# Performance work log

Measured on AMD Instinct MI355X. Metric: run time of the kernel, lower is better.

Reference implementation:

```python
import jax, jax.numpy as jnp
import numpy as np

N = 100000
F_IN = 128
HID = 64
N_CLS = 40
E = 1600000


def gcn_conv(x, src, dst, W, b, n_nodes):
    """PyG GCNConv: add self-loops, symmetric deg^{-1/2} normalization.

    Self-loop contribution handled analytically (norm_ii = 1/deg_i) so we
    never concatenate self-loop edges.
    """
    h = x @ W                                      # [N, out]
    # in-degree including self-loop
    deg = jax.ops.segment_sum(jnp.ones((src.shape[0],), x.dtype), dst,
                              num_segments=n_nodes) + 1.0
    dinv = jax.lax.rsqrt(deg)                      # deg^{-1/2}, [N]
    norm = dinv[src] * dinv[dst]                   # [E]
    msg = h[src] * norm[:, None]                   # [E, out] gather + scale
    agg = jax.ops.segment_sum(msg, dst, num_segments=n_nodes)
    return agg + h * (dinv * dinv)[:, None] + b


def setup_inputs() -> dict:
    key = jax.random.key(0)
    k1, k2, k3, k4, k5, k6 = jax.random.split(key, 6)
    x = jax.random.normal(k1, (N, F_IN), dtype=jnp.float32)
    edge_index = jax.random.randint(k2, (2, E), 0, N, dtype=jnp.int64)
    W1 = jax.random.normal(k3, (F_IN, HID), dtype=jnp.float32) / np.sqrt(F_IN)
    b1 = jnp.zeros((HID,), jnp.float32)
    W2 = jax.random.normal(k4, (HID, N_CLS), dtype=jnp.float32) / np.sqrt(HID)
    b2 = jnp.zeros((N_CLS,), jnp.float32)
    return {"x": x, "edge_index": edge_index, "W1": W1, "b1": b1,
            "W2": W2, "b2": b2}


def reference(x, edge_index, W1, b1, W2, b2):
    src, dst = edge_index[0], edge_index[1]
    h = jax.nn.relu(gcn_conv(x, src, dst, W1, b1, N))
    # dropout p=0.5 is identity at inference (training=False)
    out = gcn_conv(h, src, dst, W2, b2, N)
    return out
```

## Files before the change

kernel.cpp:

```cpp
#include <hip/hip_runtime.h>
#include <stdint.h>

#define NN    100000
#define FIN   128
#define HIDN  64
#define NCLS  40
#define NE    1600000
#define NBUCK ((NN + 255) / 256)
#define EPB   4096
#define NEB   ((NE + EPB - 1) / EPB)

typedef unsigned int uint32;
typedef __attribute__((ext_vector_type(8))) short short8v;
typedef __attribute__((ext_vector_type(4))) float f32x4;

static __device__ __forceinline__ unsigned short f2bf(float f) {
  uint32 u = __float_as_uint(f);
  u = (u + 0x7fffu + ((u >> 16) & 1u)) >> 16;
  return (unsigned short)u;
}
static __device__ __forceinline__ uint32 pack2(float lo, float hi) {
  return (uint32)f2bf(lo) | ((uint32)f2bf(hi) << 16);
}
static __device__ __forceinline__ float bf_lo(uint32 v) {
  return __uint_as_float(v << 16);
}
static __device__ __forceinline__ float bf_hi(uint32 v) {
  return __uint_as_float(v & 0xFFFF0000u);
}
static __device__ __forceinline__ f32x4 mfma_bf16(uint4 a, uint4 b, f32x4 c) {
  short8v av = __builtin_bit_cast(short8v, a);
  short8v bv = __builtin_bit_cast(short8v, b);
  return __builtin_amdgcn_mfma_f32_16x16x32_bf16(av, bv, c, 0, 0, 0);
}

static __device__ __forceinline__ int perm_col(int z) {
  return 4 * (z >> 3) + ((z & 7) >> 1) + 16 * (z & 1) + ((z >= 32) ? 16 : 0);
}

__global__ __launch_bounds__(64) void probe_kernel(const unsigned int* __restrict__ raw,
                                                   int* __restrict__ flag) {
  if (threadIdx.x == 0) {
    int is64 = 1;
    for (int i = 0; i < 64; ++i)
      if (raw[2 * i + 1] != 0u) { is64 = 0; break; }
    *flag = is64;
  }
}

__global__ __launch_bounds__(64) void wfrag_kernel(const float* __restrict__ W,
                                                   uint4* __restrict__ wfrag) {
  int idx = blockIdx.x * 64 + threadIdx.x;
  int lane = idx & 63;
  int nr = (idx >> 6) & 3;
  int kr = (idx >> 8) & 3;
  int t  = idx >> 10;
  int n  = nr * 16 + (lane & 15);
  int k0 = kr * 32 + (lane >> 4) * 8;
  uint32 w[4];
#pragma unroll
  for (int j = 0; j < 4; ++j) {
    float a = W[(k0 + 2 * j) * HIDN + n];
    float b = W[(k0 + 2 * j + 1) * HIDN + n];
    uint32 ha = f2bf(a), hb = f2bf(b);
    if (t == 0) {
      w[j] = ha | (hb << 16);
    } else {
      float ra = a - __uint_as_float(ha << 16);
      float rb = b - __uint_as_float(hb << 16);
      w[j] = (uint32)f2bf(ra) | ((uint32)f2bf(rb) << 16);
    }
  }
  wfrag[idx] = make_uint4(w[0], w[1], w[2], w[3]);
}

__global__ __launch_bounds__(256) void passA_kernel(const void* __restrict__ eptr,
                                                    const int* __restrict__ flag,
                                                    int* __restrict__ mat) {
  __shared__ int cnt[NBUCK];
  int tid = threadIdx.x;
  for (int i = tid; i < NBUCK; i += 256) cnt[i] = 0;
  __syncthreads();
  int is64 = *flag;
  int base = blockIdx.x * EPB;
#pragma unroll
  for (int k = 0; k < EPB / 256; ++k) {
    int e = base + k * 256 + tid;
    if (e < NE) {
      int d = is64 ? (int)((const long long*)eptr)[e + NE]
                   : ((const int*)eptr)[e + NE];
      atomicAdd(&cnt[d >> 8], 1);
    }
  }
  __syncthreads();
  for (int i = tid; i < NBUCK; i += 256)
    mat[blockIdx.x * NBUCK + i] = cnt[i];
}

__global__ __launch_bounds__(512) void passB1_kernel(int* __restrict__ mat,
                                                     int* __restrict__ tot) {
  __shared__ int s[512];
  int b = blockIdx.x;
  int t = threadIdx.x;
  int v = (t < NEB) ? mat[t * NBUCK + b] : 0;
  s[t] = v;
  __syncthreads();
#pragma unroll
  for (int d = 1; d < 512; d <<= 1) {
    int u = (t >= d) ? s[t - d] : 0;
    __syncthreads();
    s[t] += u;
    __syncthreads();
  }
  if (t < NEB) mat[t * NBUCK + b] = s[t] - v;
  if (t == 511) tot[b] = s[511];
}

__global__ __launch_bounds__(512) void passB2_kernel(const int* __restrict__ tot,
                                                     int* __restrict__ bbase) {
  __shared__ int s[512];
  int i = threadIdx.x;
  int v = (i < NBUCK) ? tot[i] : 0;
  s[i] = v;
  __syncthreads();
#pragma unroll
  for (int d = 1; d < 512; d <<= 1) {
    int u = (i >= d) ? s[i - d] : 0;
    __syncthreads();
    s[i] += u;
    __syncthreads();
  }
  if (i < NBUCK) bbase[i] = s[i] - v;
  if (i == 511) bbase[NBUCK] = s[511];
}

__global__ __launch_bounds__(256) void passC_kernel(const void* __restrict__ eptr,
                                                    const int* __restrict__ flag,
                                                    const int* __restrict__ mat,
                                                    const int* __restrict__ bbase,
                                                    uint32* __restrict__ bbuf) {
  __shared__ int cur[NBUCK];
  int tid = threadIdx.x;
  for (int i = tid; i < NBUCK; i += 256)
    cur[i] = bbase[i] + mat[blockIdx.x * NBUCK + i];
  __syncthreads();
  int is64 = *flag;
  int base = blockIdx.x * EPB;
#pragma unroll
  for (int k = 0; k < EPB / 256; ++k) {
    int e = base + k * 256 + tid;
    if (e < NE) {
      int s, d;
      if (is64) {
        const long long* p = (const long long*)eptr;
        s = (int)p[e]; d = (int)p[e + NE];
      } else {
        const int* p = (const int*)eptr;
        s = p[e]; d = p[e + NE];
      }
      int slot = atomicAdd(&cur[d >> 8], 1);
      bbuf[slot] = (uint32)s | ((uint32)(d & 255) << 17);
    }
  }
}

__global__ __launch_bounds__(256) void build_kernel(const int* __restrict__ bbase,
                                                    const uint32* __restrict__ bbuf,
                                                    int* __restrict__ off,
                                                    float* __restrict__ dinv,
                                                    int* __restrict__ s_src) {
  __shared__ int hist[256];
  __shared__ int lofs[256];
  __shared__ int rank[256];
  int b = blockIdx.x, tid = threadIdx.x;
  int base = bbase[b];
  int count = bbase[b + 1] - base;
  const uint32* p = bbuf + base;
  hist[tid] = 0;
  __syncthreads();
  for (int i = tid; i < count; i += 256) atomicAdd(&hist[p[i] >> 17], 1);
  __syncthreads();
  int deg = hist[tid];
  lofs[tid] = deg;
  __syncthreads();
#pragma unroll
  for (int dd = 1; dd < 256; dd <<= 1) {
    int t = (tid >= dd) ? lofs[tid - dd] : 0;
    __syncthreads();
    lofs[tid] += t;
    __syncthreads();
  }
  int excl = lofs[tid] - deg;
  __syncthreads();
  lofs[tid] = excl;
  rank[tid] = 0;
  int n = b * 256 + tid;
  if (n < NN) {
    off[n] = base + excl;
    dinv[n] = rsqrtf((float)deg + 1.0f);
  }
  if (b == 0 && tid == 0) off[NN] = NE;
  __syncthreads();
  for (int i = tid; i < count; i += 256) {
    uint32 v = p[i];
    int dl = (int)(v >> 17);
    int s = (int)(v & 0x1FFFFu);
    int r = atomicAdd(&rank[dl], 1);
    s_src[base + lofs[dl] + r] = s;
  }
}

__global__ __launch_bounds__(256) void gemm1_kernel(const float* __restrict__ x,
                                                    const uint4* __restrict__ wfrag,
                                                    const float* __restrict__ dinv,
                                                    uint32* __restrict__ hs) {
  int wid = blockIdx.x * 4 + (threadIdx.x >> 6);
  if (wid >= NN / 32) return;
  int lane = threadIdx.x & 63;
  int l15 = lane & 15, lg = lane >> 4;
  int r0 = wid * 32;
  f32x4 acc[2][4];
#pragma unroll
  for (int mr = 0; mr < 2; ++mr)
#pragma unroll
    for (int nr = 0; nr < 4; ++nr) acc[mr][nr] = (f32x4)0.f;
  const float4* x4 = (const float4*)x;
#pragma unroll
  for (int kr = 0; kr < 4; ++kr) {
    uint4 ah[2], al[2];
#pragma unroll
    for (int mr = 0; mr < 2; ++mr) {
      int m = r0 + mr * 16 + l15;
      int q0 = m * 32 + kr * 8 + lg * 2;
      float4 u = x4[q0], v = x4[q0 + 1];
      float xs[8] = {u.x, u.y, u.z, u.w, v.x, v.y, v.z, v.w};
      uint32 hw[4], lw[4];
#pragma unroll
      for (int j = 0; j < 4; ++j) {
        float a0 = xs[2 * j], a1 = xs[2 * j + 1];
        uint32 h0 = f2bf(a0), h1 = f2bf(a1);
        float ra = a0 - __uint_as_float(h0 << 16);
        float rb = a1 - __uint_as_float(h1 << 16);
        hw[j] = h0 | (h1 << 16);
        lw[j] = (uint32)f2bf(ra) | ((uint32)f2bf(rb) << 16);
      }
      ah[mr] = make_uint4(hw[0], hw[1], hw[2], hw[3]);
      al[mr] = make_uint4(lw[0], lw[1], lw[2], lw[3]);
    }
#pragma unroll
    for (int nr = 0; nr < 4; ++nr) {
      uint4 bh = wfrag[(kr * 4 + nr) * 64 + lane];
      uint4 bl = wfrag[((4 + kr) * 4 + nr) * 64 + lane];
#pragma unroll
      for (int mr = 0; mr < 2; ++mr) {
        acc[mr][nr] = mfma_bf16(ah[mr], bh, acc[mr][nr]);
        acc[mr][nr] = mfma_bf16(al[mr], bh, acc[mr][nr]);
        acc[mr][nr] = mfma_bf16(ah[mr], bl, acc[mr][nr]);
      }
    }
  }
#pragma unroll
  for (int mr = 0; mr < 2; ++mr) {
    int rb = r0 + mr * 16 + 4 * lg;
    float4 dv = *(const float4*)&dinv[rb];
#pragma unroll
    for (int a = 0; a < 2; ++a) {
#pragma unroll
      for (int j = 0; j < 4; ++j) {
        float d = (&dv.x)[j];
        uint32 wv = pack2(acc[mr][2 * a][j] * d, acc[mr][2 * a + 1][j] * d);
        hs[(size_t)(rb + j) * 32 + a * 16 + l15] = wv;
      }
    }
  }
}

__global__ __launch_bounds__(256) void agg1_kernel(const int* __restrict__ off,
                                                   const int* __restrict__ s_src,
                                                   const uint4* __restrict__ hs4,
                                                   const float* __restrict__ dinv,
                                                   const float* __restrict__ b1,
                                                   uint4* __restrict__ g) {
  int n = blockIdx.x * 4 + (threadIdx.x >> 6);
  int lane = threadIdx.x & 63;
  int q = lane >> 3;
  int hc = lane & 7;
  int j0 = off[n], j1 = off[n + 1];
  float a[8];
#pragma unroll
  for (int i = 0; i < 8; ++i) a[i] = 0.f;
  if (q == 0) {
    uint4 v = hs4[(size_t)n * 8 + hc];
    a[0] = bf_lo(v.x); a[1] = bf_hi(v.x); a[2] = bf_lo(v.y); a[3] = bf_hi(v.y);
    a[4] = bf_lo(v.z); a[5] = bf_hi(v.z); a[6] = bf_lo(v.w); a[7] = bf_hi(v.w);
  }
  int j = j0 + q;
  for (; j + 8 < j1; j += 16) {
    int sa = s_src[j], sb = s_src[j + 8];
    uint4 va = hs4[(size_t)sa * 8 + hc];
    uint4 vb = hs4[(size_t)sb * 8 + hc];
    a[0] += bf_lo(va.x); a[1] += bf_hi(va.x); a[2] += bf_lo(va.y); a[3] += bf_hi(va.y);
    a[4] += bf_lo(va.z); a[5] += bf_hi(va.z); a[6] += bf_lo(va.w); a[7] += bf_hi(va.w);
    a[0] += bf_lo(vb.x); a[1] += bf_hi(vb.x); a[2] += bf_lo(vb.y); a[3] += bf_hi(vb.y);
    a[4] += bf_lo(vb.z); a[5] += bf_hi(vb.z); a[6] += bf_lo(vb.w); a[7] += bf_hi(vb.w);
  }
  if (j < j1) {
    int sa = s_src[j];
    uint4 va = hs4[(size_t)sa * 8 + hc];
    a[0] += bf_lo(va.x); a[1] += bf_hi(va.x); a[2] += bf_lo(va.y); a[3] += bf_hi(va.y);
    a[4] += bf_lo(va.z); a[5] += bf_hi(va.z); a[6] += bf_lo(va.w); a[7] += bf_hi(va.w);
  }
#pragma unroll
  for (int i = 0; i < 8; ++i) {
    a[i] += __shfl_xor(a[i], 8, 64);
    a[i] += __shfl_xor(a[i], 16, 64);
    a[i] += __shfl_xor(a[i], 32, 64);
  }
  if (q == 0) {
    float di = dinv[n];
    float bb[8];
#pragma unroll
    for (int i = 0; i < 8; ++i)
      bb[i] = b1[perm_col(hc * 8 + i)];
    float r0 = di * fmaxf(a[0] * di + bb[0], 0.f);
    float r1 = di * fmaxf(a[1] * di + bb[1], 0.f);
    float r2 = di * fmaxf(a[2] * di + bb[2], 0.f);
    float r3 = di * fmaxf(a[3] * di + bb[3], 0.f);
    float r4 = di * fmaxf(a[4] * di + bb[4], 0.f);
    float r5 = di * fmaxf(a[5] * di + bb[5], 0.f);
    float r6 = di * fmaxf(a[6] * di + bb[6], 0.f);
    float r7 = di * fmaxf(a[7] * di + bb[7], 0.f);
    uint4 o;
    o.x = pack2(r0, r1); o.y = pack2(r2, r3);
    o.z = pack2(r4, r5); o.w = pack2(r6, r7);
    g[(size_t)n * 8 + hc] = o;
  }
}

__global__ __launch_bounds__(256) void agg2_kernel(const int* __restrict__ off,
                                                   const int* __restrict__ s_src,
                                                   const uint4* __restrict__ g,
                                                   const float* __restrict__ dinv,
                                                   float* __restrict__ t) {
  int n = blockIdx.x * 4 + (threadIdx.x >> 6);
  int lane = threadIdx.x & 63;
  int q = lane >> 3;
  int hc = lane & 7;
  int j0 = off[n], j1 = off[n + 1];
  float a[8];
#pragma unroll
  for (int i = 0; i < 8; ++i) a[i] = 0.f;
  if (q == 0) {
    uint4 v = g[(size_t)n * 8 + hc];
    a[0] = bf_lo(v.x); a[1] = bf_hi(v.x); a[2] = bf_lo(v.y); a[3] = bf_hi(v.y);
    a[4] = bf_lo(v.z); a[5] = bf_hi(v.z); a[6] = bf_lo(v.w); a[7] = bf_hi(v.w);
  }
  int j = j0 + q;
  for (; j + 8 < j1; j += 16) {
    int sa = s_src[j], sb = s_src[j + 8];
    uint4 va = g[(size_t)sa * 8 + hc];
    uint4 vb = g[(size_t)sb * 8 + hc];
    a[0] += bf_lo(va.x); a[1] += bf_hi(va.x); a[2] += bf_lo(va.y); a[3] += bf_hi(va.y);
    a[4] += bf_lo(va.z); a[5] += bf_hi(va.z); a[6] += bf_lo(va.w); a[7] += bf_hi(va.w);
    a[0] += bf_lo(vb.x); a[1] += bf_hi(vb.x); a[2] += bf_lo(vb.y); a[3] += bf_hi(vb.y);
    a[4] += bf_lo(vb.z); a[5] += bf_hi(vb.z); a[6] += bf_lo(vb.w); a[7] += bf_hi(vb.w);
  }
  if (j < j1) {
    int sa = s_src[j];
    uint4 va = g[(size_t)sa * 8 + hc];
    a[0] += bf_lo(va.x); a[1] += bf_hi(va.x); a[2] += bf_lo(va.y); a[3] += bf_hi(va.y);
    a[4] += bf_lo(va.z); a[5] += bf_hi(va.z); a[6] += bf_lo(va.w); a[7] += bf_hi(va.w);
  }
#pragma unroll
  for (int i = 0; i < 8; ++i) {
    a[i] += __shfl_xor(a[i], 8, 64);
    a[i] += __shfl_xor(a[i], 16, 64);
    a[i] += __shfl_xor(a[i], 32, 64);
  }
  if (q == 0) {
    float di = dinv[n];
    float* tp = &t[(size_t)n * HIDN + hc * 8];
    *(float4*)tp = make_float4(a[0] * di, a[1] * di, a[2] * di, a[3] * di);
    *(float4*)(tp + 4) = make_float4(a[4] * di, a[5] * di, a[6] * di, a[7] * di);
  }
}

__global__ __launch_bounds__(256) void mv_kernel(const float* __restrict__ t,
                                                 const float* __restrict__ W2,
                                                 const float* __restrict__ b2,
                                                 float* __restrict__ out) {
  __shared__ float sW[HIDN * NCLS];
  int tid = threadIdx.x;
  for (int i = tid; i < HIDN * (NCLS / 4); i += 256) {
    int z = i / 10, j = i - z * 10;
    int c = perm_col(z);
    ((float4*)sW)[z * 10 + j] = ((const float4*)W2)[c * 10 + j];
  }
  __syncthreads();
  int cg = tid & 1;
  int r = blockIdx.x * 128 + (tid >> 1);
  if (r >= NN) return;
  int c0 = cg * 20;
  float acc[20];
#pragma unroll
  for (int j = 0; j < 20; ++j) acc[j] = b2[c0 + j];
  const float4* t4 = (const float4*)(t + (size_t)r * HIDN);
#pragma unroll 4
  for (int k4 = 0; k4 < 16; ++k4) {
    float4 tv = t4[k4];
#pragma unroll
    for (int kk = 0; kk < 4; ++kk) {
      float xv = (&tv.x)[kk];
      const float* wr = &sW[(k4 * 4 + kk) * NCLS + c0];
#pragma unroll
      for (int j = 0; j < 5; ++j) {
        float4 wv = *(const float4*)&wr[j * 4];
        acc[j * 4 + 0] = fmaf(xv, wv.x, acc[j * 4 + 0]);
        acc[j * 4 + 1] = fmaf(xv, wv.y, acc[j * 4 + 1]);
        acc[j * 4 + 2] = fmaf(xv, wv.z, acc[j * 4 + 2]);
        acc[j * 4 + 3] = fmaf(xv, wv.w, acc[j * 4 + 3]);
      }
    }
  }
  float4* op = (float4*)&out[(size_t)r * NCLS + c0];
#pragma unroll
  for (int j = 0; j < 5; ++j)
    op[j] = make_float4(acc[j * 4 + 0], acc[j * 4 + 1],
                        acc[j * 4 + 2], acc[j * 4 + 3]);
}

extern "C" void kernel_launch(void* const* d_in, const int* in_sizes, int n_in,
                              void* d_out, int out_size, void* d_ws, size_t ws_size,
                              hipStream_t stream) {
  const float* x  = (const float*)d_in[0];
  const void*  ei = d_in[1];
  const float* W1 = (const float*)d_in[2];
  const float* b1 = (const float*)d_in[3];
  const float* W2 = (const float*)d_in[4];
  const float* b2 = (const float*)d_in[5];
  float* out = (float*)d_out;

  char* w = (char*)d_ws;
  size_t off_b = 0;
  auto carve = [&](size_t bytes) -> void* {
    void* p = w + off_b;
    off_b = (off_b + bytes + 255) & ~(size_t)255;
    return p;
  };
  int*    mat   = (int*)   carve((size_t)NEB * NBUCK * 4);
  int*    tot   = (int*)   carve((size_t)NBUCK * 4);
  int*    bbase = (int*)   carve((size_t)(NBUCK + 1) * 4);
  int*    offs  = (int*)   carve((size_t)(NN + 1) * 4);
  float*  dinv  = (float*) carve((size_t)NN * 4);
  int*    flag  = (int*)   carve(256);
  int*    s_src = (int*)   carve((size_t)NE * 4);
  uint32* hs    = (uint32*)carve((size_t)NN * 32 * 4);
  uint4*  g     = (uint4*) carve((size_t)NN * 8 * 16);
  float*  t     = (float*) carve((size_t)NN * HIDN * 4);
  uint32* bbuf  = (uint32*)carve((size_t)NE * 4);
  uint4*  wfrag = (uint4*) carve((size_t)2048 * 16);

  probe_kernel<<<1, 64, 0, stream>>>((const unsigned int*)ei, flag);
  wfrag_kernel<<<32, 64, 0, stream>>>(W1, wfrag);
  passA_kernel<<<NEB, 256, 0, stream>>>(ei, flag, mat);
  passB1_kernel<<<NBUCK, 512, 0, stream>>>(mat, tot);
  passB2_kernel<<<1, 512, 0, stream>>>(tot, bbase);
  passC_kernel<<<NEB, 256, 0, stream>>>(ei, flag, mat, bbase, bbuf);
  build_kernel<<<NBUCK, 256, 0, stream>>>(bbase, bbuf, offs, dinv, s_src);
  gemm1_kernel<<<(NN / 32 + 3) / 4, 256, 0, stream>>>(x, wfrag, dinv, hs);
  agg1_kernel<<<NN / 4, 256, 0, stream>>>(offs, s_src, (const uint4*)hs, dinv, b1, g);
  agg2_kernel<<<NN / 4, 256, 0, stream>>>(offs, s_src, g, dinv, t);
  mv_kernel<<<(NN + 127) / 128, 256, 0, stream>>>(t, W2, b2, out);
}
```

Measured before the change: 262.0 us.

## Assign one 8-lane group per node in aggregation kernels instead of a wavefront

The two aggregation kernels now map 8 lanes to each destination node, so a block covers 32 nodes instead of 4 and one lane walks the whole neighbor list serially. This removes the cross-lane shuffle reduction and the idle lanes left by the old 64-lanes-per-node layout, where most lanes had little work at an average degree of about 16. The layer-1 bias is permuted once inside wfrag_kernel so agg1 can read it with vector loads. In exchange each lane now has a longer serial chain of dependent gathers, and high-degree nodes can cause more load imbalance within a wavefront.

```diff
diff --git a/kernel.cpp b/kernel.cpp
--- a/kernel.cpp
+++ b/kernel.cpp
@@ -49,8 +49,11 @@
 }
 
 __global__ __launch_bounds__(64) void wfrag_kernel(const float* __restrict__ W,
-                                                   uint4* __restrict__ wfrag) {
+                                                   const float* __restrict__ b1,
+                                                   uint4* __restrict__ wfrag,
+                                                   float* __restrict__ b1p) {
   int idx = blockIdx.x * 64 + threadIdx.x;
+  if (idx < 64) b1p[idx] = b1[perm_col(idx)];
   int lane = idx & 63;
   int nr = (idx >> 6) & 3;
   int kr = (idx >> 8) & 3;
@@ -279,24 +282,21 @@
                                                    const int* __restrict__ s_src,
                                                    const uint4* __restrict__ hs4,
                                                    const float* __restrict__ dinv,
-                                                   const float* __restrict__ b1,
+                                                   const float* __restrict__ b1p,
                                                    uint4* __restrict__ g) {
-  int n = blockIdx.x * 4 + (threadIdx.x >> 6);
-  int lane = threadIdx.x & 63;
-  int q = lane >> 3;
-  int hc = lane & 7;
+  int tid = threadIdx.x;
+  int n = blockIdx.x * 32 + (tid >> 3);
+  int hc = tid & 7;
   int j0 = off[n], j1 = off[n + 1];
   float a[8];
-#pragma unroll
-  for (int i = 0; i < 8; ++i) a[i] = 0.f;
-  if (q == 0) {
+  {
     uint4 v = hs4[(size_t)n * 8 + hc];
     a[0] = bf_lo(v.x); a[1] = bf_hi(v.x); a[2] = bf_lo(v.y); a[3] = bf_hi(v.y);
     a[4] = bf_lo(v.z); a[5] = bf_hi(v.z); a[6] = bf_lo(v.w); a[7] = bf_hi(v.w);
   }
-  int j = j0 + q;
-  for (; j + 8 < j1; j += 16) {
-    int sa = s_src[j], sb = s_src[j + 8];
+  int j = j0;
+  for (; j + 1 < j1; j += 2) {
+    int sa = s_src[j], sb = s_src[j + 1];
     uint4 va = hs4[(size_t)sa * 8 + hc];
     uint4 vb = hs4[(size_t)sb * 8 + hc];
     a[0] += bf_lo(va.x); a[1] += bf_hi(va.x); a[2] += bf_lo(va.y); a[3] += bf_hi(va.y);
@@ -310,31 +310,21 @@
     a[0] += bf_lo(va.x); a[1] += bf_hi(va.x); a[2] += bf_lo(va.y); a[3] += bf_hi(va.y);
     a[4] += bf_lo(va.z); a[5] += bf_hi(va.z); a[6] += bf_lo(va.w); a[7] += bf_hi(va.w);
   }
-#pragma unroll
-  for (int i = 0; i < 8; ++i) {
-    a[i] += __shfl_xor(a[i], 8, 64);
-    a[i] += __shfl_xor(a[i], 16, 64);
-    a[i] += __shfl_xor(a[i], 32, 64);
-  }
-  if (q == 0) {
-    float di = dinv[n];
-    float bb[8];
-#pragma unroll
-    for (int i = 0; i < 8; ++i)
-      bb[i] = b1[perm_col(hc * 8 + i)];
-    float r0 = di * fmaxf(a[0] * di + bb[0], 0.f);
-    float r1 = di * fmaxf(a[1] * di + bb[1], 0.f);
-    float r2 = di * fmaxf(a[2] * di + bb[2], 0.f);
-    float r3 = di * fmaxf(a[3] * di + bb[3], 0.f);
-    float r4 = di * fmaxf(a[4] * di + bb[4], 0.f);
-    float r5 = di * fmaxf(a[5] * di + bb[5], 0.f);
-    float r6 = di * fmaxf(a[6] * di + bb[6], 0.f);
-    float r7 = di * fmaxf(a[7] * di + bb[7], 0.f);
-    uint4 o;
-    o.x = pack2(r0, r1); o.y = pack2(r2, r3);
-    o.z = pack2(r4, r5); o.w = pack2(r6, r7);
-    g[(size_t)n * 8 + hc] = o;
-  }
+  float di = dinv[n];
+  float4 b0 = *(const float4*)&b1p[hc * 8];
+  float4 b4 = *(const float4*)&b1p[hc * 8 + 4];
+  float r0 = di * fmaxf(a[0] * di + b0.x, 0.f);
+  float r1 = di * fmaxf(a[1] * di + b0.y, 0.f);
+  float r2 = di * fmaxf(a[2] * di + b0.z, 0.f);
+  float r3 = di * fmaxf(a[3] * di + b0.w, 0.f);
+  float r4 = di * fmaxf(a[4] * di + b4.x, 0.f);
+  float r5 = di * fmaxf(a[5] * di + b4.y, 0.f);
+  float r6 = di * fmaxf(a[6] * di + b4.z, 0.f);
+  float r7 = di * fmaxf(a[7] * di + b4.w, 0.f);
+  uint4 o;
+  o.x = pack2(r0, r1); o.y = pack2(r2, r3);
+  o.z = pack2(r4, r5); o.w = pack2(r6, r7);
+  g[(size_t)n * 8 + hc] = o;
 }
 
 __global__ __launch_bounds__(256) void agg2_kernel(const int* __restrict__ off,
@@ -342,22 +332,19 @@
                                                    const uint4* __restrict__ g,
                                                    const float* __restrict__ dinv,
                                                    float* __restrict__ t) {
-  int n = blockIdx.x * 4 + (threadIdx.x >> 6);
-  int lane = threadIdx.x & 63;
-  int q = lane >> 3;
-  int hc = lane & 7;
+  int tid = threadIdx.x;
+  int n = blockIdx.x * 32 + (tid >> 3);
+  int hc = tid & 7;
   int j0 = off[n], j1 = off[n + 1];
   float a[8];
-#pragma unroll
-  for (int i = 0; i < 8; ++i) a[i] = 0.f;
-  if (q == 0) {
+  {
     uint4 v = g[(size_t)n * 8 + hc];
     a[0] = bf_lo(v.x); a[1] = bf_hi(v.x); a[2] = bf_lo(v.y); a[3] = bf_hi(v.y);
     a[4] = bf_lo(v.z); a[5] = bf_hi(v.z); a[6] = bf_lo(v.w); a[7] = bf_hi(v.w);
   }
-  int j = j0 + q;
-  for (; j + 8 < j1; j += 16) {
-    int sa = s_src[j], sb = s_src[j + 8];
+  int j = j0;
+  for (; j + 1 < j1; j += 2) {
+    int sa = s_src[j], sb = s_src[j + 1];
     uint4 va = g[(size_t)sa * 8 + hc];
     uint4 vb = g[(size_t)sb * 8 + hc];
     a[0] += bf_lo(va.x); a[1] += bf_hi(va.x); a[2] += bf_lo(va.y); a[3] += bf_hi(va.y);
@@ -371,18 +358,10 @@
     a[0] += bf_lo(va.x); a[1] += bf_hi(va.x); a[2] += bf_lo(va.y); a[3] += bf_hi(va.y);
     a[4] += bf_lo(va.z); a[5] += bf_hi(va.z); a[6] += bf_lo(va.w); a[7] += bf_hi(va.w);
   }
-#pragma unroll
-  for (int i = 0; i < 8; ++i) {
-    a[i] += __shfl_xor(a[i], 8, 64);
-    a[i] += __shfl_xor(a[i], 16, 64);
-    a[i] += __shfl_xor(a[i], 32, 64);
-  }
-  if (q == 0) {
-    float di = dinv[n];
-    float* tp = &t[(size_t)n * HIDN + hc * 8];
-    *(float4*)tp = make_float4(a[0] * di, a[1] * di, a[2] * di, a[3] * di);
-    *(float4*)(tp + 4) = make_float4(a[4] * di, a[5] * di, a[6] * di, a[7] * di);
-  }
+  float di = dinv[n];
+  float* tp = &t[(size_t)n * HIDN + hc * 8];
+  *(float4*)tp = make_float4(a[0] * di, a[1] * di, a[2] * di, a[3] * di);
+  *(float4*)(tp + 4) = make_float4(a[4] * di, a[5] * di, a[6] * di, a[7] * di);
 }
 
 __global__ __launch_bounds__(256) void mv_kernel(const float* __restrict__ t,
@@ -459,16 +438,17 @@
   float*  t     = (float*) carve((size_t)NN * HIDN * 4);
   uint32* bbuf  = (uint32*)carve((size_t)NE * 4);
   uint4*  wfrag = (uint4*) carve((size_t)2048 * 16);
+  float*  b1p   = (float*) carve((size_t)HIDN * 4);
 
   probe_kernel<<<1, 64, 0, stream>>>((const unsigned int*)ei, flag);
-  wfrag_kernel<<<32, 64, 0, stream>>>(W1, wfrag);
+  wfrag_kernel<<<32, 64, 0, stream>>>(W1, b1, wfrag, b1p);
   passA_kernel<<<NEB, 256, 0, stream>>>(ei, flag, mat);
   passB1_kernel<<<NBUCK, 512, 0, stream>>>(mat, tot);
   passB2_kernel<<<1, 512, 0, stream>>>(tot, bbase);
   passC_kernel<<<NEB, 256, 0, stream>>>(ei, flag, mat, bbase, bbuf);
   build_kernel<<<NBUCK, 256, 0, stream>>>(bbase, bbuf, offs, dinv, s_src);
   gemm1_kernel<<<(NN / 32 + 3) / 4, 256, 0, stream>>>(x, wfrag, dinv, hs);
-  agg1_kernel<<<NN / 4, 256, 0, stream>>>(offs, s_src, (const uint4*)hs, dinv, b1, g);
-  agg2_kernel<<<NN / 4, 256, 0, stream>>>(offs, s_src, g, dinv, t);
+  agg1_kernel<<<NN / 32, 256, 0, stream>>>(offs, s_src, (const uint4*)hs, dinv, b1p, g);
+  agg2_kernel<<<NN / 32, 256, 0, stream>>>(offs, s_src, g, dinv, t);
   mv_kernel<<<(NN + 127) / 128, 256, 0, stream>>>(t, W2, b2, out);
 }
```

Result: faster. 247.1 us (-5.7%).
